# Kernel optimization log

Measured on AMD Instinct MI355X. Metric: run time of the kernel, lower is better.

The kernel has to match this reference:

```python
import jax, jax.numpy as jnp
import numpy as np

N, X_DIM, Z_DIM, H = 4096, 256, 128, 512
NUM_ACTIONS = 4
TEMPERATURE = 0.1


def _init_linear(key, fan_in, fan_out):
    kw, kb = jax.random.split(key)
    bound = 1.0 / np.sqrt(fan_in)
    W = jax.random.uniform(kw, (fan_in, fan_out), minval=-bound, maxval=bound, dtype=jnp.float32)
    b = jax.random.uniform(kb, (fan_out,), minval=-bound, maxval=bound, dtype=jnp.float32)
    return W, b


def setup_inputs() -> dict:
    key = jax.random.key(0)
    ks = jax.random.split(key, 9)
    s = jax.random.normal(ks[0], (N, X_DIM), dtype=jnp.float32)
    sp = jax.random.normal(ks[1], (N, X_DIM), dtype=jnp.float32)
    a = jax.random.randint(ks[2], (N,), 0, NUM_ACTIONS)
    a1h = jax.nn.one_hot(a, NUM_ACTIONS, dtype=jnp.float32)
    # phi: x_dim -> 512 -> 512 -> z_dim
    pW0, pb0 = _init_linear(ks[3], X_DIM, H)
    pW1, pb1 = _init_linear(ks[4], H, H)
    pW2, pb2 = _init_linear(ks[5], H, Z_DIM)
    # g: x_dim + 4 -> 512 -> 512 -> z_dim
    gW0, gb0 = _init_linear(ks[6], X_DIM + NUM_ACTIONS, H)
    gW1, gb1 = _init_linear(ks[7], H, H)
    gW2, gb2 = _init_linear(ks[8], H, Z_DIM)
    return {"s": s, "sp": sp, "a1h": a1h,
            "pW0": pW0, "pb0": pb0, "pW1": pW1, "pb1": pb1, "pW2": pW2, "pb2": pb2,
            "gW0": gW0, "gb0": gb0, "gW1": gW1, "gb1": gb1, "gW2": gW2, "gb2": gb2}


def _mlp(x, W0, b0, W1, b1, W2, b2):
    h = jax.nn.relu(x @ W0 + b0)
    h = jax.nn.relu(h @ W1 + b1)
    return h @ W2 + b2


def reference(s, sp, a1h, pW0, pb0, pW1, pb1, pW2, pb2, gW0, gb0, gW1, gb1, gW2, gb2):
    z = _mlp(s, pW0, pb0, pW1, pb1, pW2, pb2)                      # [N, D]
    zpos = _mlp(jnp.concatenate([sp, a1h], axis=-1), gW0, gb0, gW1, gb1, gW2, gb2)  # [N, D]
    # -||z_i - zpos_j||^2 / T via the GEMM trick (avoids the [N,N,D] diff tensor)
    sq_z = jnp.sum(z * z, axis=-1, keepdims=True)                  # [N, 1]
    sq_p = jnp.sum(zpos * zpos, axis=-1)                            # [N]
    logits = -(sq_z + sq_p[None, :] - 2.0 * z @ zpos.T) / TEMPERATURE  # [N, N]
    # cross-entropy with targets = arange(N): diagonal is the positive
    log_probs = jax.nn.log_softmax(logits, axis=-1)
    loss = -jnp.mean(jnp.diagonal(log_probs))
    return loss
```

## Files before the change

### kernel.cpp

```cpp
#include <hip/hip_runtime.h>
#include <math.h>

#define NR 4096
#define ZD 128
#define HD 512
#define NJR 32
#define INV_T 10.0f

typedef __attribute__((ext_vector_type(8))) short bf16x8;
typedef __attribute__((ext_vector_type(4))) short short4v;
typedef __attribute__((ext_vector_type(4))) float f32x4;

typedef const unsigned int __attribute__((address_space(1)))* gas_t;
typedef unsigned int __attribute__((address_space(3)))* las_t;

__device__ __forceinline__ unsigned short f2bf(float f) {
  union { float f; unsigned u; } v; v.f = f;
  unsigned r = v.u + 0x7fff + ((v.u >> 16) & 1);
  return (unsigned short)(r >> 16);
}
__device__ __forceinline__ float bf2f(unsigned short b) {
  union { unsigned u; float f; } v; v.u = ((unsigned)b) << 16;
  return v.f;
}


__global__ __launch_bounds__(256) void prep(
    const float* __restrict__ s, const float* __restrict__ sp,
    const float* __restrict__ a1h,
    unsigned short* __restrict__ Sb, unsigned short* __restrict__ SPb,
    int* __restrict__ aidx,
    const float* __restrict__ pW0, unsigned short* __restrict__ pW0t,
    const float* __restrict__ pW1, unsigned short* __restrict__ pW1t,
    const float* __restrict__ pW2, unsigned short* __restrict__ pW2t,
    const float* __restrict__ gW0, unsigned short* __restrict__ gW0t,
    const float* __restrict__ gW1, unsigned short* __restrict__ gW1t,
    const float* __restrict__ gW2, unsigned short* __restrict__ gW2t,
    float* __restrict__ out) {
  int b = blockIdx.x, tid = threadIdx.x;
  if (b < 16) {
    int r = b * 256 + tid;
    int a = 0;
#pragma unroll
    for (int j = 0; j < 4; ++j) if (a1h[(size_t)r * 4 + j] > 0.5f) a = j;
    aidx[r] = a;
    if (b == 0 && tid == 0) out[0] = 0.f;
    return;
  }
  const int idx8 = tid & 127;
  const int h = idx8 & 1, p = idx8 >> 1, hi = p >> 4, l15 = p & 15;
  if (b < 2064) {
    const float* src = (b < 1040) ? s : sp;
    unsigned short* dst = (b < 1040) ? Sb : SPb;
    int lb = (b < 1040) ? b - 16 : b - 1040;
    int s0 = lb * 2 + (tid >> 7);
    int rf = s0 >> 3, ks = s0 & 7;
    int row = rf * 16 + l15, c0 = ks * 32 + hi * 4 + h * 16;
    float4 v = *(const float4*)&src[(size_t)row * 256 + c0];
    short4v o = { (short)f2bf(v.x), (short)f2bf(v.y), (short)f2bf(v.z), (short)f2bf(v.w) };
    *(short4v*)((char*)dst + (size_t)s0 * 1024 + idx8 * 8) = o;
    return;
  }
  int local = b - 2064;
  const float* W; unsigned short* Wt; int N, ksh;
  if (local < 128)      { W = pW0; Wt = pW0t; N = 512; ksh = 3; }
  else if (local < 384) { W = pW1; Wt = pW1t; N = 512; ksh = 4; local -= 128; }
  else if (local < 448) { W = pW2; Wt = pW2t; N = 128; ksh = 4; local -= 384; }
  else if (local < 576) { W = gW0; Wt = gW0t; N = 512; ksh = 3; local -= 448; }
  else if (local < 832) { W = gW1; Wt = gW1t; N = 512; ksh = 4; local -= 576; }
  else                  { W = gW2; Wt = gW2t; N = 128; ksh = 4; local -= 832; }
  int s0 = local * 2 + (tid >> 7);
  int rf = s0 >> ksh, ks = s0 & ((1 << ksh) - 1);
  int n = rf * 16 + l15, k0 = ks * 32 + hi * 4 + h * 16;
  short4v o = { (short)f2bf(W[(size_t)(k0 + 0) * N + n]),
                (short)f2bf(W[(size_t)(k0 + 1) * N + n]),
                (short)f2bf(W[(size_t)(k0 + 2) * N + n]),
                (short)f2bf(W[(size_t)(k0 + 3) * N + n]) };
  *(short4v*)((char*)Wt + (size_t)s0 * 1024 + idx8 * 8) = o;
}

template <int BM, int K, bool RELU, bool GB, bool SQ>
__global__ __launch_bounds__(256) void gemm_p3(
    const unsigned short* __restrict__ A0, const unsigned short* __restrict__ A1,
    const unsigned short* __restrict__ W0, const unsigned short* __restrict__ W1,
    const float* __restrict__ b0, const float* __restrict__ b1,
    unsigned short* __restrict__ C0, unsigned short* __restrict__ C1,
    float* __restrict__ sqp2, int N,
    const int* __restrict__ aidx, const float* __restrict__ gW0f) {
  constexpr int KS = K >> 5;
  constexpr int NSTEP = K >> 6;
  constexpr int ABYTES = BM * 128;
  constexpr int BBYTES = 8192;
  constexpr int NA = BM >> 5;
  constexpr int WM_FR = BM >> 5;
  constexpr int V = NA + 2;
  __shared__ char lds[3 * (ABYTES + BBYTES)];
  char* AsB = lds;
  char* BsB = lds + 3 * ABYTES;

  const int tid = threadIdx.x, lane = tid & 63, w = tid >> 6;
  const int wm = w >> 1, wn = w & 1;
  const int z = blockIdx.z;
  const char* Ab = (const char*)(z ? A1 : A0);
  const char* Wb = (const char*)(z ? W1 : W0);
  const float* bias = z ? b1 : b0;
  char* Cb = (char*)(z ? C1 : C0);
  const int bm = blockIdx.x * BM, bn = blockIdx.y * 64;
  const int lane16 = lane * 16;

  auto stage = [&](int buf, int st) {
#pragma unroll
    for (int u = 0; u < NA; ++u) {
      const int sl = w * NA + u;
      const char* src = Ab + ((size_t)((bm >> 4) + (sl >> 1)) * KS + st * 2 + (sl & 1)) * 1024 + lane16;
      __builtin_amdgcn_global_load_lds((gas_t)src, (las_t)(AsB + buf * ABYTES + sl * 1024), 16, 0, 0);
    }
#pragma unroll
    for (int u = 0; u < 2; ++u) {
      const int sl = w * 2 + u;
      const char* src = Wb + ((size_t)((bn >> 4) + (sl >> 1)) * KS + st * 2 + (sl & 1)) * 1024 + lane16;
      __builtin_amdgcn_global_load_lds((gas_t)src, (las_t)(BsB + buf * BBYTES + sl * 1024), 16, 0, 0);
    }
  };

  f32x4 acc[WM_FR][2] = {};
  stage(0, 0);
  stage(1, 1);
#pragma unroll
  for (int st = 0; st < NSTEP; ++st) {
    const int buf = st % 3;
    if (st + 2 < NSTEP) {
      stage((st + 2) % 3, st + 2);
      if constexpr (V == 6) asm volatile("s_waitcnt vmcnt(12)" ::: "memory");
      else                  asm volatile("s_waitcnt vmcnt(8)" ::: "memory");
    } else if (st + 1 < NSTEP) {
      if constexpr (V == 6) asm volatile("s_waitcnt vmcnt(6)" ::: "memory");
      else                  asm volatile("s_waitcnt vmcnt(4)" ::: "memory");
    } else {
      asm volatile("s_waitcnt vmcnt(0)" ::: "memory");
    }
    __builtin_amdgcn_s_barrier();
#pragma unroll
    for (int kss = 0; kss < 2; ++kss) {
      bf16x8 af[WM_FR], bfv[2];
#pragma unroll
      for (int i = 0; i < WM_FR; ++i)
        af[i] = *(const bf16x8*)(AsB + buf * ABYTES + ((wm * WM_FR + i) * 2 + kss) * 1024 + lane16);
#pragma unroll
      for (int j = 0; j < 2; ++j)
        bfv[j] = *(const bf16x8*)(BsB + buf * BBYTES + ((wn * 2 + j) * 2 + kss) * 1024 + lane16);
#pragma unroll
      for (int i = 0; i < WM_FR; ++i)
#pragma unroll
        for (int j = 0; j < 2; ++j)
          acc[i][j] = __builtin_amdgcn_mfma_f32_16x16x32_bf16(bfv[j], af[i], acc[i][j], 0, 0, 0);
    }
    __builtin_amdgcn_s_barrier();
  }

  const int l15 = lane & 15, hi = lane >> 4;
  const int NS = N >> 5;
  const int row0 = bm + wm * (BM / 2);
  const int col0 = bn + wn * 32;
  float sq[WM_FR];
  int ar[WM_FR];
#pragma unroll
  for (int i = 0; i < WM_FR; ++i) { sq[i] = 0.f; ar[i] = 0; }
  if (GB && z == 1) {
#pragma unroll
    for (int i = 0; i < WM_FR; ++i) ar[i] = aidx[row0 + i * 16 + l15];
  }
  float4 bi0 = *(const float4*)&bias[col0 + hi * 4];
  float4 bi1 = *(const float4*)&bias[col0 + 16 + hi * 4];
#pragma unroll
  for (int i = 0; i < WM_FR; ++i) {
    const int rfC = (row0 >> 4) + i;
    float v[8] = { acc[i][0][0] + bi0.x, acc[i][0][1] + bi0.y,
                   acc[i][0][2] + bi0.z, acc[i][0][3] + bi0.w,
                   acc[i][1][0] + bi1.x, acc[i][1][1] + bi1.y,
                   acc[i][1][2] + bi1.z, acc[i][1][3] + bi1.w };
    if (GB && z == 1) {
      float4 g0 = *(const float4*)&gW0f[(size_t)(256 + ar[i]) * N + col0 + hi * 4];
      float4 g1 = *(const float4*)&gW0f[(size_t)(256 + ar[i]) * N + col0 + 16 + hi * 4];
      v[0] += g0.x; v[1] += g0.y; v[2] += g0.z; v[3] += g0.w;
      v[4] += g1.x; v[5] += g1.y; v[6] += g1.z; v[7] += g1.w;
    }
    bf16x8 r;
#pragma unroll
    for (int t = 0; t < 8; ++t) {
      float vv = RELU ? fmaxf(v[t], 0.f) : v[t];
      unsigned short cv = f2bf(vv);
      r[t] = (short)cv;
      if (SQ) { float vb = bf2f(cv); sq[i] += vb * vb; }
    }
    *(bf16x8*)(Cb + (size_t)(rfC * NS + (col0 >> 5)) * 1024 + lane16) = r;
  }
  if (SQ && z == 1) {
#pragma unroll
    for (int i = 0; i < WM_FR; ++i) {
      float t = sq[i];
      t += __shfl_xor(t, 16, 64);
      t += __shfl_xor(t, 32, 64);
      if (lane < 16) sqp2[(size_t)(col0 >> 5) * NR + row0 + i * 16 + lane] = t;
    }
  }
}

__global__ __launch_bounds__(256) void logits_fm(
    const unsigned short* __restrict__ Zb, const unsigned short* __restrict__ Zpb,
    const float* __restrict__ sqp2, float* __restrict__ wm_,
    float* __restrict__ wsum, float* __restrict__ wdiag) {
  const int tid = threadIdx.x, lane = tid & 63, w = tid >> 6;
  const int l15 = lane & 15, hi = lane >> 4;
  const int i0 = blockIdx.x * 128, jr = blockIdx.y;
  const int row32 = i0 + w * 32;
  const int jbase = jr * 128;
  const int lane16 = lane * 16;
  const char* Zc = (const char*)Zb;
  const char* Pc = (const char*)Zpb;

  bf16x8 afr[2][4];
#pragma unroll
  for (int rf = 0; rf < 2; ++rf)
#pragma unroll
    for (int ks = 0; ks < 4; ++ks)
      afr[rf][ks] = *(const bf16x8*)(Zc + (size_t)(((row32 >> 4) + rf) * 4 + ks) * 1024 + lane16);

  f32x4 acc[2][8] = {};
#pragma unroll
  for (int jf = 0; jf < 8; ++jf) {
    const size_t js = (size_t)((jbase >> 4) + jf) * 4;
#pragma unroll
    for (int ks = 0; ks < 4; ++ks) {
      bf16x8 bfv = *(const bf16x8*)(Pc + (js + ks) * 1024 + lane16);
      acc[0][jf] = __builtin_amdgcn_mfma_f32_16x16x32_bf16(bfv, afr[0][ks], acc[0][jf], 0, 0, 0);
      acc[1][jf] = __builtin_amdgcn_mfma_f32_16x16x32_bf16(bfv, afr[1][ks], acc[1][jf], 0, 0, 0);
    }
  }

#pragma unroll
  for (int rf = 0; rf < 2; ++rf) {
    const int grow = row32 + rf * 16 + l15;
    float mx = -INFINITY, dd = 0.f;
    bool hasd = false;
#pragma unroll
    for (int jf = 0; jf < 8; ++jf) {
      const int cb = jbase + jf * 16 + hi * 4;
      float4 q0 = *(const float4*)&sqp2[cb];
      float4 q1 = *(const float4*)&sqp2[NR + cb];
      float4 q2 = *(const float4*)&sqp2[2 * NR + cb];
      float4 q3 = *(const float4*)&sqp2[3 * NR + cb];
      float sp[4] = { q0.x + q1.x + q2.x + q3.x, q0.y + q1.y + q2.y + q3.y,
                      q0.z + q1.z + q2.z + q3.z, q0.w + q1.w + q2.w + q3.w };
#pragma unroll
      for (int e = 0; e < 4; ++e) {
        float lv = (2.f * acc[rf][jf][e] - sp[e]) * INV_T;
        acc[rf][jf][e] = lv;
        mx = fmaxf(mx, lv);
        if (cb + e == grow) { dd = lv; hasd = true; }
      }
    }
    mx = fmaxf(mx, __shfl_xor(mx, 16, 64));
    mx = fmaxf(mx, __shfl_xor(mx, 32, 64));
    float sum = 0.f;
#pragma unroll
    for (int jf = 0; jf < 8; ++jf)
#pragma unroll
      for (int e = 0; e < 4; ++e) sum += __expf(acc[rf][jf][e] - mx);
    sum += __shfl_xor(sum, 16, 64);
    sum += __shfl_xor(sum, 32, 64);
    if (hi == 0) {
      wm_[(size_t)jr * NR + grow] = mx;
      wsum[(size_t)jr * NR + grow] = sum;
    }
    if (hasd) wdiag[grow] = dd;
  }
}

__global__ __launch_bounds__(256) void finalize(const float* __restrict__ wm,
    const float* __restrict__ wsum, const float* __restrict__ wdiag,
    float* __restrict__ out) {
  int r = blockIdx.x * 256 + threadIdx.x;
  float mm = wm[r];
  float ss = wsum[r];
#pragma unroll
  for (int p = 1; p < NJR; ++p) {
    float mo = wm[(size_t)p * NR + r];
    float so = wsum[(size_t)p * NR + r];
    float mn = fmaxf(mm, mo);
    ss = ss * __expf(mm - mn) + so * __expf(mo - mn);
    mm = mn;
  }
  float loss_r = mm + logf(ss) - wdiag[r];
  float v = loss_r;
#pragma unroll
  for (int off = 32; off; off >>= 1) v += __shfl_xor(v, off, 64);
  __shared__ float partial[4];
  if ((threadIdx.x & 63) == 0) partial[threadIdx.x >> 6] = v;
  __syncthreads();
  if (threadIdx.x == 0)
    atomicAdd(out, (partial[0] + partial[1] + partial[2] + partial[3]) * (1.0f / (float)NR));
}

extern "C" void kernel_launch(void* const* d_in, const int* in_sizes, int n_in,
                              void* d_out, int out_size, void* d_ws, size_t ws_size,
                              hipStream_t stream) {
  const float* s   = (const float*)d_in[0];
  const float* sp  = (const float*)d_in[1];
  const float* a1h = (const float*)d_in[2];
  const float* pW0 = (const float*)d_in[3];
  const float* pb0 = (const float*)d_in[4];
  const float* pW1 = (const float*)d_in[5];
  const float* pb1 = (const float*)d_in[6];
  const float* pW2 = (const float*)d_in[7];
  const float* pb2 = (const float*)d_in[8];
  const float* gW0 = (const float*)d_in[9];
  const float* gb0 = (const float*)d_in[10];
  const float* gW1 = (const float*)d_in[11];
  const float* gb1 = (const float*)d_in[12];
  const float* gW2 = (const float*)d_in[13];
  const float* gb2 = (const float*)d_in[14];

  char* p = (char*)d_ws;
  unsigned short* Sb   = (unsigned short*)p; p += (size_t)NR * 256 * 2;
  unsigned short* SPb  = (unsigned short*)p; p += (size_t)NR * 256 * 2;
  unsigned short* H1   = (unsigned short*)p; p += (size_t)2 * NR * HD * 2;
  unsigned short* H2   = (unsigned short*)p; p += (size_t)2 * NR * HD * 2;
  unsigned short* Zall = (unsigned short*)p; p += (size_t)2 * NR * ZD * 2;
  unsigned short* pW0t = (unsigned short*)p; p += (size_t)256 * 512 * 2;
  unsigned short* pW1t = (unsigned short*)p; p += (size_t)512 * 512 * 2;
  unsigned short* pW2t = (unsigned short*)p; p += (size_t)512 * 128 * 2;
  unsigned short* gW0t = (unsigned short*)p; p += (size_t)256 * 512 * 2;
  unsigned short* gW1t = (unsigned short*)p; p += (size_t)512 * 512 * 2;
  unsigned short* gW2t = (unsigned short*)p; p += (size_t)512 * 128 * 2;
  float* sqp2 = (float*)p; p += (size_t)4 * NR * 4;
  float* wm   = (float*)p; p += (size_t)NJR * NR * 4;
  float* wsm  = (float*)p; p += (size_t)NJR * NR * 4;
  float* wdg  = (float*)p; p += (size_t)NR * 4;
  int*   aidx = (int*)p;  p += (size_t)NR * 4;

  unsigned short* H1g = H1 + (size_t)NR * HD;
  unsigned short* H2g = H2 + (size_t)NR * HD;
  unsigned short* Zb  = Zall;
  unsigned short* Zpb = Zall + (size_t)NR * ZD;

  dim3 blk(256);
  prep<<<2960, blk, 0, stream>>>(s, sp, a1h, Sb, SPb, aidx,
                                 pW0, pW0t, pW1, pW1t, pW2, pW2t,
                                 gW0, gW0t, gW1, gW1t, gW2, gW2t,
                                 (float*)d_out);

  gemm_p3<128, 256, true, true, false><<<dim3(32, 8, 2), blk, 0, stream>>>(
      Sb, SPb, pW0t, gW0t, pb0, gb0, H1, H1g, nullptr, 512, aidx, gW0);
  gemm_p3<128, 512, true, false, false><<<dim3(32, 8, 2), blk, 0, stream>>>(
      H1, H1g, pW1t, gW1t, pb1, gb1, H2, H2g, nullptr, 512, nullptr, nullptr);
  gemm_p3<64, 512, false, false, true><<<dim3(64, 2, 2), blk, 0, stream>>>(
      H2, H2g, pW2t, gW2t, pb2, gb2, Zb, Zpb, sqp2, 128, nullptr, nullptr);

  logits_fm<<<dim3(NR / 128, NJR), blk, 0, stream>>>(Zb, Zpb, sqp2, wm, wsm, wdg);
  finalize<<<NR / 256, blk, 0, stream>>>(wm, wsm, wdg, (float*)d_out);
}
```

Measured before the change: 54.47 us.

## Fuse three MLP GEMM layers into one kernel keeping hidden activations in LDS

Replaces the three per-layer GEMM launches with a single kernel in which each block processes 32 rows through all three layers. Hidden activations stay in shared memory instead of round-tripping through global H1/H2 buffers. Weights are streamed directly from global memory into registers with one-step register prefetch instead of the LDS triple-buffered pipeline. This removes launch overhead and intermediate global traffic, but every block rereads the full weight matrices from global/L2, with 256 blocks and larger per-wave register footprint.

```diff
diff --git a/kernel.cpp b/kernel.cpp
--- a/kernel.cpp
+++ b/kernel.cpp
@@ -2,7 +2,6 @@
 #include <math.h>
 
 #define NR 4096
-#define ZD 128
 #define HD 512
 #define NJR 32
 #define INV_T 10.0f
@@ -10,9 +9,6 @@
 typedef __attribute__((ext_vector_type(8))) short bf16x8;
 typedef __attribute__((ext_vector_type(4))) short short4v;
 typedef __attribute__((ext_vector_type(4))) float f32x4;
-
-typedef const unsigned int __attribute__((address_space(1)))* gas_t;
-typedef unsigned int __attribute__((address_space(3)))* las_t;
 
 __device__ __forceinline__ unsigned short f2bf(float f) {
   union { float f; unsigned u; } v; v.f = f;
@@ -79,129 +75,191 @@
   *(short4v*)((char*)Wt + (size_t)s0 * 1024 + idx8 * 8) = o;
 }
 
-template <int BM, int K, bool RELU, bool GB, bool SQ>
-__global__ __launch_bounds__(256) void gemm_p3(
-    const unsigned short* __restrict__ A0, const unsigned short* __restrict__ A1,
-    const unsigned short* __restrict__ W0, const unsigned short* __restrict__ W1,
-    const float* __restrict__ b0, const float* __restrict__ b1,
-    unsigned short* __restrict__ C0, unsigned short* __restrict__ C1,
-    float* __restrict__ sqp2, int N,
-    const int* __restrict__ aidx, const float* __restrict__ gW0f) {
-  constexpr int KS = K >> 5;
-  constexpr int NSTEP = K >> 6;
-  constexpr int ABYTES = BM * 128;
-  constexpr int BBYTES = 8192;
-  constexpr int NA = BM >> 5;
-  constexpr int WM_FR = BM >> 5;
-  constexpr int V = NA + 2;
-  __shared__ char lds[3 * (ABYTES + BBYTES)];
-  char* AsB = lds;
-  char* BsB = lds + 3 * ABYTES;
-
-  const int tid = threadIdx.x, lane = tid & 63, w = tid >> 6;
-  const int wm = w >> 1, wn = w & 1;
-  const int z = blockIdx.z;
-  const char* Ab = (const char*)(z ? A1 : A0);
-  const char* Wb = (const char*)(z ? W1 : W0);
-  const float* bias = z ? b1 : b0;
-  char* Cb = (char*)(z ? C1 : C0);
-  const int bm = blockIdx.x * BM, bn = blockIdx.y * 64;
+__global__ __launch_bounds__(256) void mlp_fused(
+    const unsigned short* __restrict__ Sb, const unsigned short* __restrict__ SPb,
+    const unsigned short* __restrict__ pW0t, const unsigned short* __restrict__ pW1t,
+    const unsigned short* __restrict__ pW2t,
+    const unsigned short* __restrict__ gW0t, const unsigned short* __restrict__ gW1t,
+    const unsigned short* __restrict__ gW2t,
+    const float* __restrict__ pb0, const float* __restrict__ pb1,
+    const float* __restrict__ pb2,
+    const float* __restrict__ gb0, const float* __restrict__ gb1,
+    const float* __restrict__ gb2,
+    unsigned short* __restrict__ Zb, unsigned short* __restrict__ Zpb,
+    float* __restrict__ sqp2, const int* __restrict__ aidx,
+    const float* __restrict__ gW0f) {
+  __shared__ __align__(1024) char Hs[32768];
+  const int tid = threadIdx.x, lane = tid & 63, wn = tid >> 6;
+  const int l15 = lane & 15, hi = lane >> 4;
+  const int z = blockIdx.y;
+  const int bm = blockIdx.x * 32;
   const int lane16 = lane * 16;
-
-  auto stage = [&](int buf, int st) {
-#pragma unroll
-    for (int u = 0; u < NA; ++u) {
-      const int sl = w * NA + u;
-      const char* src = Ab + ((size_t)((bm >> 4) + (sl >> 1)) * KS + st * 2 + (sl & 1)) * 1024 + lane16;
-      __builtin_amdgcn_global_load_lds((gas_t)src, (las_t)(AsB + buf * ABYTES + sl * 1024), 16, 0, 0);
-    }
-#pragma unroll
-    for (int u = 0; u < 2; ++u) {
-      const int sl = w * 2 + u;
-      const char* src = Wb + ((size_t)((bn >> 4) + (sl >> 1)) * KS + st * 2 + (sl & 1)) * 1024 + lane16;
-      __builtin_amdgcn_global_load_lds((gas_t)src, (las_t)(BsB + buf * BBYTES + sl * 1024), 16, 0, 0);
-    }
-  };
-
-  f32x4 acc[WM_FR][2] = {};
-  stage(0, 0);
-  stage(1, 1);
-#pragma unroll
-  for (int st = 0; st < NSTEP; ++st) {
-    const int buf = st % 3;
-    if (st + 2 < NSTEP) {
-      stage((st + 2) % 3, st + 2);
-      if constexpr (V == 6) asm volatile("s_waitcnt vmcnt(12)" ::: "memory");
-      else                  asm volatile("s_waitcnt vmcnt(8)" ::: "memory");
-    } else if (st + 1 < NSTEP) {
-      if constexpr (V == 6) asm volatile("s_waitcnt vmcnt(6)" ::: "memory");
-      else                  asm volatile("s_waitcnt vmcnt(4)" ::: "memory");
-    } else {
-      asm volatile("s_waitcnt vmcnt(0)" ::: "memory");
-    }
-    __builtin_amdgcn_s_barrier();
-#pragma unroll
-    for (int kss = 0; kss < 2; ++kss) {
-      bf16x8 af[WM_FR], bfv[2];
-#pragma unroll
-      for (int i = 0; i < WM_FR; ++i)
-        af[i] = *(const bf16x8*)(AsB + buf * ABYTES + ((wm * WM_FR + i) * 2 + kss) * 1024 + lane16);
-#pragma unroll
-      for (int j = 0; j < 2; ++j)
-        bfv[j] = *(const bf16x8*)(BsB + buf * BBYTES + ((wn * 2 + j) * 2 + kss) * 1024 + lane16);
-#pragma unroll
-      for (int i = 0; i < WM_FR; ++i)
-#pragma unroll
-        for (int j = 0; j < 2; ++j)
-          acc[i][j] = __builtin_amdgcn_mfma_f32_16x16x32_bf16(bfv[j], af[i], acc[i][j], 0, 0, 0);
-    }
-    __builtin_amdgcn_s_barrier();
-  }
-
-  const int l15 = lane & 15, hi = lane >> 4;
-  const int NS = N >> 5;
-  const int row0 = bm + wm * (BM / 2);
-  const int col0 = bn + wn * 32;
-  float sq[WM_FR];
-  int ar[WM_FR];
-#pragma unroll
-  for (int i = 0; i < WM_FR; ++i) { sq[i] = 0.f; ar[i] = 0; }
-  if (GB && z == 1) {
-#pragma unroll
-    for (int i = 0; i < WM_FR; ++i) ar[i] = aidx[row0 + i * 16 + l15];
-  }
-  float4 bi0 = *(const float4*)&bias[col0 + hi * 4];
-  float4 bi1 = *(const float4*)&bias[col0 + 16 + hi * 4];
-#pragma unroll
-  for (int i = 0; i < WM_FR; ++i) {
-    const int rfC = (row0 >> 4) + i;
-    float v[8] = { acc[i][0][0] + bi0.x, acc[i][0][1] + bi0.y,
-                   acc[i][0][2] + bi0.z, acc[i][0][3] + bi0.w,
-                   acc[i][1][0] + bi1.x, acc[i][1][1] + bi1.y,
-                   acc[i][1][2] + bi1.z, acc[i][1][3] + bi1.w };
-    if (GB && z == 1) {
-      float4 g0 = *(const float4*)&gW0f[(size_t)(256 + ar[i]) * N + col0 + hi * 4];
-      float4 g1 = *(const float4*)&gW0f[(size_t)(256 + ar[i]) * N + col0 + 16 + hi * 4];
-      v[0] += g0.x; v[1] += g0.y; v[2] += g0.z; v[3] += g0.w;
-      v[4] += g1.x; v[5] += g1.y; v[6] += g1.z; v[7] += g1.w;
-    }
-    bf16x8 r;
-#pragma unroll
-    for (int t = 0; t < 8; ++t) {
-      float vv = RELU ? fmaxf(v[t], 0.f) : v[t];
-      unsigned short cv = f2bf(vv);
-      r[t] = (short)cv;
-      if (SQ) { float vb = bf2f(cv); sq[i] += vb * vb; }
-    }
-    *(bf16x8*)(Cb + (size_t)(rfC * NS + (col0 >> 5)) * 1024 + lane16) = r;
-  }
-  if (SQ && z == 1) {
-#pragma unroll
-    for (int i = 0; i < WM_FR; ++i) {
-      float t = sq[i];
-      t += __shfl_xor(t, 16, 64);
-      t += __shfl_xor(t, 32, 64);
-      if (lane < 16) sqp2[(size_t)(col0 >> 5) * NR + row0 + i * 16 + lane] = t;
+  const char* Ab  = (const char*)(z ? SPb : Sb);
+  const char* W0b = (const char*)(z ? gW0t : pW0t);
+  const char* W1b = (const char*)(z ? gW1t : pW1t);
+  const char* W2b = (const char*)(z ? gW2t : pW2t);
+  const float* b0 = z ? gb0 : pb0;
+  const float* b1 = z ? gb1 : pb1;
+  const float* b2 = z ? gb2 : pb2;
+  char* Cb = (char*)(z ? Zpb : Zb);
+
+  int ar[2];
+  ar[0] = aidx[bm + l15];
+  ar[1] = aidx[bm + 16 + l15];
+
+  {
+    f32x4 acc[2][8] = {};
+    bf16x8 bcur[8], acur[2];
+#pragma unroll
+    for (int jf = 0; jf < 8; ++jf)
+      bcur[jf] = *(const bf16x8*)(W0b + (size_t)((wn * 8 + jf) * 8) * 1024 + lane16);
+#pragma unroll
+    for (int rf = 0; rf < 2; ++rf)
+      acur[rf] = *(const bf16x8*)(Ab + (size_t)(((bm >> 4) + rf) * 8) * 1024 + lane16);
+#pragma unroll
+    for (int ks = 0; ks < 8; ++ks) {
+      bf16x8 bnx[8], anx[2];
+      if (ks < 7) {
+#pragma unroll
+        for (int jf = 0; jf < 8; ++jf)
+          bnx[jf] = *(const bf16x8*)(W0b + (size_t)((wn * 8 + jf) * 8 + ks + 1) * 1024 + lane16);
+#pragma unroll
+        for (int rf = 0; rf < 2; ++rf)
+          anx[rf] = *(const bf16x8*)(Ab + (size_t)(((bm >> 4) + rf) * 8 + ks + 1) * 1024 + lane16);
+      }
+#pragma unroll
+      for (int rf = 0; rf < 2; ++rf)
+#pragma unroll
+        for (int jf = 0; jf < 8; ++jf)
+          acc[rf][jf] = __builtin_amdgcn_mfma_f32_16x16x32_bf16(bcur[jf], acur[rf], acc[rf][jf], 0, 0, 0);
+      if (ks < 7) {
+#pragma unroll
+        for (int jf = 0; jf < 8; ++jf) bcur[jf] = bnx[jf];
+        acur[0] = anx[0]; acur[1] = anx[1];
+      }
+    }
+#pragma unroll
+    for (int rf = 0; rf < 2; ++rf)
+#pragma unroll
+      for (int q = 0; q < 4; ++q) {
+        const int col0 = wn * 128 + q * 32;
+        float4 bi0 = *(const float4*)&b0[col0 + hi * 4];
+        float4 bi1 = *(const float4*)&b0[col0 + 16 + hi * 4];
+        float v[8] = { acc[rf][2 * q][0] + bi0.x, acc[rf][2 * q][1] + bi0.y,
+                       acc[rf][2 * q][2] + bi0.z, acc[rf][2 * q][3] + bi0.w,
+                       acc[rf][2 * q + 1][0] + bi1.x, acc[rf][2 * q + 1][1] + bi1.y,
+                       acc[rf][2 * q + 1][2] + bi1.z, acc[rf][2 * q + 1][3] + bi1.w };
+        if (z == 1) {
+          float4 g0 = *(const float4*)&gW0f[(size_t)(256 + ar[rf]) * 512 + col0 + hi * 4];
+          float4 g1 = *(const float4*)&gW0f[(size_t)(256 + ar[rf]) * 512 + col0 + 16 + hi * 4];
+          v[0] += g0.x; v[1] += g0.y; v[2] += g0.z; v[3] += g0.w;
+          v[4] += g1.x; v[5] += g1.y; v[6] += g1.z; v[7] += g1.w;
+        }
+        bf16x8 r;
+#pragma unroll
+        for (int t = 0; t < 8; ++t) r[t] = (short)f2bf(fmaxf(v[t], 0.f));
+        *(bf16x8*)(Hs + ((rf * 16 + wn * 4 + q) * 1024) + lane16) = r;
+      }
+  }
+  __syncthreads();
+
+  {
+    f32x4 acc[2][8] = {};
+    bf16x8 bcur[8];
+#pragma unroll
+    for (int jf = 0; jf < 8; ++jf)
+      bcur[jf] = *(const bf16x8*)(W1b + (size_t)((wn * 8 + jf) * 16) * 1024 + lane16);
+#pragma unroll
+    for (int ks = 0; ks < 16; ++ks) {
+      bf16x8 bnx[8];
+      if (ks < 15) {
+#pragma unroll
+        for (int jf = 0; jf < 8; ++jf)
+          bnx[jf] = *(const bf16x8*)(W1b + (size_t)((wn * 8 + jf) * 16 + ks + 1) * 1024 + lane16);
+      }
+      bf16x8 a0 = *(const bf16x8*)(Hs + ((0 * 16 + ks) * 1024) + lane16);
+      bf16x8 a1 = *(const bf16x8*)(Hs + ((1 * 16 + ks) * 1024) + lane16);
+#pragma unroll
+      for (int jf = 0; jf < 8; ++jf) {
+        acc[0][jf] = __builtin_amdgcn_mfma_f32_16x16x32_bf16(bcur[jf], a0, acc[0][jf], 0, 0, 0);
+        acc[1][jf] = __builtin_amdgcn_mfma_f32_16x16x32_bf16(bcur[jf], a1, acc[1][jf], 0, 0, 0);
+      }
+      if (ks < 15) {
+#pragma unroll
+        for (int jf = 0; jf < 8; ++jf) bcur[jf] = bnx[jf];
+      }
+    }
+    __syncthreads();
+#pragma unroll
+    for (int rf = 0; rf < 2; ++rf)
+#pragma unroll
+      for (int q = 0; q < 4; ++q) {
+        const int col0 = wn * 128 + q * 32;
+        float4 bi0 = *(const float4*)&b1[col0 + hi * 4];
+        float4 bi1 = *(const float4*)&b1[col0 + 16 + hi * 4];
+        float v[8] = { acc[rf][2 * q][0] + bi0.x, acc[rf][2 * q][1] + bi0.y,
+                       acc[rf][2 * q][2] + bi0.z, acc[rf][2 * q][3] + bi0.w,
+                       acc[rf][2 * q + 1][0] + bi1.x, acc[rf][2 * q + 1][1] + bi1.y,
+                       acc[rf][2 * q + 1][2] + bi1.z, acc[rf][2 * q + 1][3] + bi1.w };
+        bf16x8 r;
+#pragma unroll
+        for (int t = 0; t < 8; ++t) r[t] = (short)f2bf(fmaxf(v[t], 0.f));
+        *(bf16x8*)(Hs + ((rf * 16 + wn * 4 + q) * 1024) + lane16) = r;
+      }
+  }
+  __syncthreads();
+
+  {
+    f32x4 acc[2][2] = {};
+    bf16x8 bcur[2];
+#pragma unroll
+    for (int fn = 0; fn < 2; ++fn)
+      bcur[fn] = *(const bf16x8*)(W2b + (size_t)((wn * 2 + fn) * 16) * 1024 + lane16);
+#pragma unroll
+    for (int ks = 0; ks < 16; ++ks) {
+      bf16x8 bnx[2];
+      if (ks < 15) {
+#pragma unroll
+        for (int fn = 0; fn < 2; ++fn)
+          bnx[fn] = *(const bf16x8*)(W2b + (size_t)((wn * 2 + fn) * 16 + ks + 1) * 1024 + lane16);
+      }
+      bf16x8 a0 = *(const bf16x8*)(Hs + ((0 * 16 + ks) * 1024) + lane16);
+      bf16x8 a1 = *(const bf16x8*)(Hs + ((1 * 16 + ks) * 1024) + lane16);
+#pragma unroll
+      for (int fn = 0; fn < 2; ++fn) {
+        acc[0][fn] = __builtin_amdgcn_mfma_f32_16x16x32_bf16(bcur[fn], a0, acc[0][fn], 0, 0, 0);
+        acc[1][fn] = __builtin_amdgcn_mfma_f32_16x16x32_bf16(bcur[fn], a1, acc[1][fn], 0, 0, 0);
+      }
+      if (ks < 15) { bcur[0] = bnx[0]; bcur[1] = bnx[1]; }
+    }
+    const int col0 = wn * 32;
+    float4 bi0 = *(const float4*)&b2[col0 + hi * 4];
+    float4 bi1 = *(const float4*)&b2[col0 + 16 + hi * 4];
+    float sq[2] = {0.f, 0.f};
+#pragma unroll
+    for (int rf = 0; rf < 2; ++rf) {
+      float v[8] = { acc[rf][0][0] + bi0.x, acc[rf][0][1] + bi0.y,
+                     acc[rf][0][2] + bi0.z, acc[rf][0][3] + bi0.w,
+                     acc[rf][1][0] + bi1.x, acc[rf][1][1] + bi1.y,
+                     acc[rf][1][2] + bi1.z, acc[rf][1][3] + bi1.w };
+      bf16x8 r;
+#pragma unroll
+      for (int t = 0; t < 8; ++t) {
+        unsigned short cv = f2bf(v[t]);
+        r[t] = (short)cv;
+        float vb = bf2f(cv);
+        sq[rf] += vb * vb;
+      }
+      *(bf16x8*)(Cb + (size_t)((((bm >> 4) + rf) * 4 + wn) * 1024) + lane16) = r;
+    }
+    if (z == 1) {
+#pragma unroll
+      for (int rf = 0; rf < 2; ++rf) {
+        float t = sq[rf];
+        t += __shfl_xor(t, 16, 64);
+        t += __shfl_xor(t, 32, 64);
+        if (lane < 16) sqp2[(size_t)wn * NR + bm + rf * 16 + lane] = t;
+      }
     }
   }
 }
@@ -324,9 +382,7 @@
   char* p = (char*)d_ws;
   unsigned short* Sb   = (unsigned short*)p; p += (size_t)NR * 256 * 2;
   unsigned short* SPb  = (unsigned short*)p; p += (size_t)NR * 256 * 2;
-  unsigned short* H1   = (unsigned short*)p; p += (size_t)2 * NR * HD * 2;
-  unsigned short* H2   = (unsigned short*)p; p += (size_t)2 * NR * HD * 2;
-  unsigned short* Zall = (unsigned short*)p; p += (size_t)2 * NR * ZD * 2;
+  unsigned short* Zall = (unsigned short*)p; p += (size_t)2 * NR * 128 * 2;
   unsigned short* pW0t = (unsigned short*)p; p += (size_t)256 * 512 * 2;
   unsigned short* pW1t = (unsigned short*)p; p += (size_t)512 * 512 * 2;
   unsigned short* pW2t = (unsigned short*)p; p += (size_t)512 * 128 * 2;
@@ -339,10 +395,8 @@
   float* wdg  = (float*)p; p += (size_t)NR * 4;
   int*   aidx = (int*)p;  p += (size_t)NR * 4;
 
-  unsigned short* H1g = H1 + (size_t)NR * HD;
-  unsigned short* H2g = H2 + (size_t)NR * HD;
   unsigned short* Zb  = Zall;
-  unsigned short* Zpb = Zall + (size_t)NR * ZD;
+  unsigned short* Zpb = Zall + (size_t)NR * 128;
 
   dim3 blk(256);
   prep<<<2960, blk, 0, stream>>>(s, sp, a1h, Sb, SPb, aidx,
@@ -350,12 +404,10 @@
                                  gW0, gW0t, gW1, gW1t, gW2, gW2t,
                                  (float*)d_out);
 
-  gemm_p3<128, 256, true, true, false><<<dim3(32, 8, 2), blk, 0, stream>>>(
-      Sb, SPb, pW0t, gW0t, pb0, gb0, H1, H1g, nullptr, 512, aidx, gW0);
-  gemm_p3<128, 512, true, false, false><<<dim3(32, 8, 2), blk, 0, stream>>>(
-      H1, H1g, pW1t, gW1t, pb1, gb1, H2, H2g, nullptr, 512, nullptr, nullptr);
-  gemm_p3<64, 512, false, false, true><<<dim3(64, 2, 2), blk, 0, stream>>>(
-      H2, H2g, pW2t, gW2t, pb2, gb2, Zb, Zpb, sqp2, 128, nullptr, nullptr);
+  mlp_fused<<<dim3(NR / 32, 2), blk, 0, stream>>>(
+      Sb, SPb, pW0t, pW1t, pW2t, gW0t, gW1t, gW2t,
+      pb0, pb1, pb2, gb0, gb1, gb2,
+      Zb, Zpb, sqp2, aidx, gW0);
 
   logits_fm<<<dim3(NR / 128, NJR), blk, 0, stream>>>(Zb, Zpb, sqp2, wm, wsm, wdg);
   finalize<<<NR / 256, blk, 0, stream>>>(wm, wsm, wdg, (float*)d_out);
```

Measured after the change: 71.19 us. 30.7% more time.

## Switch MLP GEMMs to smaller double-buffered tiles and atomic squared-norm accumulation

Applied to the files above, without the earlier changes.

The MLP GEMM kernel now uses generic BM/BN tiles with double buffering in place of triple buffering. Layers 0 and 1 drop from 128x64 to 64x64 tiles and layer 2 from 64x64 to 64x32, doubling the block count per launch to improve occupancy and wave balance. The per-column-slab squared-norm partials are replaced by atomicAdd into one zeroed array, so the logits kernel reads one value per column instead of summing four. The trade-off is less data reuse per tile, a shallower prefetch pipeline, and atomic contention on the norm buffer.

```diff
diff --git a/kernel.cpp b/kernel.cpp
--- a/kernel.cpp
+++ b/kernel.cpp
@@ -2,7 +2,6 @@
 #include <math.h>
 
 #define NR 4096
-#define ZD 128
 #define HD 512
 #define NJR 32
 #define INV_T 10.0f
@@ -29,7 +28,7 @@
     const float* __restrict__ s, const float* __restrict__ sp,
     const float* __restrict__ a1h,
     unsigned short* __restrict__ Sb, unsigned short* __restrict__ SPb,
-    int* __restrict__ aidx,
+    int* __restrict__ aidx, float* __restrict__ sqp,
     const float* __restrict__ pW0, unsigned short* __restrict__ pW0t,
     const float* __restrict__ pW1, unsigned short* __restrict__ pW1t,
     const float* __restrict__ pW2, unsigned short* __restrict__ pW2t,
@@ -44,6 +43,7 @@
 #pragma unroll
     for (int j = 0; j < 4; ++j) if (a1h[(size_t)r * 4 + j] > 0.5f) a = j;
     aidx[r] = a;
+    sqp[r] = 0.f;
     if (b == 0 && tid == 0) out[0] = 0.f;
     return;
   }
@@ -79,24 +79,24 @@
   *(short4v*)((char*)Wt + (size_t)s0 * 1024 + idx8 * 8) = o;
 }
 
-template <int BM, int K, bool RELU, bool GB, bool SQ>
-__global__ __launch_bounds__(256) void gemm_p3(
+template <int BM, int BN, int K, bool RELU, bool GB, bool SQ>
+__global__ __launch_bounds__(256) void gemm_db(
     const unsigned short* __restrict__ A0, const unsigned short* __restrict__ A1,
     const unsigned short* __restrict__ W0, const unsigned short* __restrict__ W1,
     const float* __restrict__ b0, const float* __restrict__ b1,
     unsigned short* __restrict__ C0, unsigned short* __restrict__ C1,
-    float* __restrict__ sqp2, int N,
+    float* __restrict__ sqp, int N,
     const int* __restrict__ aidx, const float* __restrict__ gW0f) {
   constexpr int KS = K >> 5;
   constexpr int NSTEP = K >> 6;
-  constexpr int ABYTES = BM * 128;
-  constexpr int BBYTES = 8192;
-  constexpr int NA = BM >> 5;
-  constexpr int WM_FR = BM >> 5;
-  constexpr int V = NA + 2;
-  __shared__ char lds[3 * (ABYTES + BBYTES)];
-  char* AsB = lds;
-  char* BsB = lds + 3 * ABYTES;
+  constexpr int ABY = BM * 128;
+  constexpr int BBY = BN * 128;
+  constexpr int RFW = BM >> 5;
+  constexpr int FNW = BN >> 5;
+  constexpr int V = RFW + FNW;
+  __shared__ char lds[2 * (ABY + BBY)];
+  char* As = lds;
+  char* Bs = lds + 2 * ABY;
 
   const int tid = threadIdx.x, lane = tid & 63, w = tid >> 6;
   const int wm = w >> 1, wn = w & 1;
@@ -105,54 +105,50 @@
   const char* Wb = (const char*)(z ? W1 : W0);
   const float* bias = z ? b1 : b0;
   char* Cb = (char*)(z ? C1 : C0);
-  const int bm = blockIdx.x * BM, bn = blockIdx.y * 64;
+  const int bm = blockIdx.x * BM, bn = blockIdx.y * BN;
   const int lane16 = lane * 16;
 
   auto stage = [&](int buf, int st) {
 #pragma unroll
-    for (int u = 0; u < NA; ++u) {
-      const int sl = w * NA + u;
+    for (int u = 0; u < RFW; ++u) {
+      const int sl = w * RFW + u;
       const char* src = Ab + ((size_t)((bm >> 4) + (sl >> 1)) * KS + st * 2 + (sl & 1)) * 1024 + lane16;
-      __builtin_amdgcn_global_load_lds((gas_t)src, (las_t)(AsB + buf * ABYTES + sl * 1024), 16, 0, 0);
-    }
-#pragma unroll
-    for (int u = 0; u < 2; ++u) {
-      const int sl = w * 2 + u;
+      __builtin_amdgcn_global_load_lds((gas_t)src, (las_t)(As + buf * ABY + sl * 1024), 16, 0, 0);
+    }
+#pragma unroll
+    for (int u = 0; u < FNW; ++u) {
+      const int sl = w * FNW + u;
       const char* src = Wb + ((size_t)((bn >> 4) + (sl >> 1)) * KS + st * 2 + (sl & 1)) * 1024 + lane16;
-      __builtin_amdgcn_global_load_lds((gas_t)src, (las_t)(BsB + buf * BBYTES + sl * 1024), 16, 0, 0);
+      __builtin_amdgcn_global_load_lds((gas_t)src, (las_t)(Bs + buf * BBY + sl * 1024), 16, 0, 0);
     }
   };
 
-  f32x4 acc[WM_FR][2] = {};
+  f32x4 acc[RFW][FNW] = {};
   stage(0, 0);
-  stage(1, 1);
 #pragma unroll
   for (int st = 0; st < NSTEP; ++st) {
-    const int buf = st % 3;
-    if (st + 2 < NSTEP) {
-      stage((st + 2) % 3, st + 2);
-      if constexpr (V == 6) asm volatile("s_waitcnt vmcnt(12)" ::: "memory");
-      else                  asm volatile("s_waitcnt vmcnt(8)" ::: "memory");
-    } else if (st + 1 < NSTEP) {
-      if constexpr (V == 6) asm volatile("s_waitcnt vmcnt(6)" ::: "memory");
-      else                  asm volatile("s_waitcnt vmcnt(4)" ::: "memory");
+    const int buf = st & 1;
+    if (st + 1 < NSTEP) {
+      stage(buf ^ 1, st + 1);
+      if constexpr (V == 4) asm volatile("s_waitcnt vmcnt(4)" ::: "memory");
+      else                  asm volatile("s_waitcnt vmcnt(3)" ::: "memory");
     } else {
       asm volatile("s_waitcnt vmcnt(0)" ::: "memory");
     }
     __builtin_amdgcn_s_barrier();
 #pragma unroll
     for (int kss = 0; kss < 2; ++kss) {
-      bf16x8 af[WM_FR], bfv[2];
-#pragma unroll
-      for (int i = 0; i < WM_FR; ++i)
-        af[i] = *(const bf16x8*)(AsB + buf * ABYTES + ((wm * WM_FR + i) * 2 + kss) * 1024 + lane16);
-#pragma unroll
-      for (int j = 0; j < 2; ++j)
-        bfv[j] = *(const bf16x8*)(BsB + buf * BBYTES + ((wn * 2 + j) * 2 + kss) * 1024 + lane16);
-#pragma unroll
-      for (int i = 0; i < WM_FR; ++i)
-#pragma unroll
-        for (int j = 0; j < 2; ++j)
+      bf16x8 af[RFW], bfv[FNW];
+#pragma unroll
+      for (int i = 0; i < RFW; ++i)
+        af[i] = *(const bf16x8*)(As + buf * ABY + ((wm * RFW + i) * 2 + kss) * 1024 + lane16);
+#pragma unroll
+      for (int j = 0; j < FNW; ++j)
+        bfv[j] = *(const bf16x8*)(Bs + buf * BBY + ((wn * FNW + j) * 2 + kss) * 1024 + lane16);
+#pragma unroll
+      for (int i = 0; i < RFW; ++i)
+#pragma unroll
+        for (int j = 0; j < FNW; ++j)
           acc[i][j] = __builtin_amdgcn_mfma_f32_16x16x32_bf16(bfv[j], af[i], acc[i][j], 0, 0, 0);
     }
     __builtin_amdgcn_s_barrier();
@@ -160,55 +156,74 @@
 
   const int l15 = lane & 15, hi = lane >> 4;
   const int NS = N >> 5;
-  const int row0 = bm + wm * (BM / 2);
-  const int col0 = bn + wn * 32;
-  float sq[WM_FR];
-  int ar[WM_FR];
-#pragma unroll
-  for (int i = 0; i < WM_FR; ++i) { sq[i] = 0.f; ar[i] = 0; }
+  const int row0 = bm + wm * (RFW * 16);
+  const int col0 = bn + wn * (FNW * 16);
+  int ar[RFW];
+#pragma unroll
+  for (int i = 0; i < RFW; ++i) ar[i] = 0;
   if (GB && z == 1) {
 #pragma unroll
-    for (int i = 0; i < WM_FR; ++i) ar[i] = aidx[row0 + i * 16 + l15];
-  }
-  float4 bi0 = *(const float4*)&bias[col0 + hi * 4];
-  float4 bi1 = *(const float4*)&bias[col0 + 16 + hi * 4];
-#pragma unroll
-  for (int i = 0; i < WM_FR; ++i) {
-    const int rfC = (row0 >> 4) + i;
-    float v[8] = { acc[i][0][0] + bi0.x, acc[i][0][1] + bi0.y,
-                   acc[i][0][2] + bi0.z, acc[i][0][3] + bi0.w,
-                   acc[i][1][0] + bi1.x, acc[i][1][1] + bi1.y,
-                   acc[i][1][2] + bi1.z, acc[i][1][3] + bi1.w };
-    if (GB && z == 1) {
-      float4 g0 = *(const float4*)&gW0f[(size_t)(256 + ar[i]) * N + col0 + hi * 4];
-      float4 g1 = *(const float4*)&gW0f[(size_t)(256 + ar[i]) * N + col0 + 16 + hi * 4];
-      v[0] += g0.x; v[1] += g0.y; v[2] += g0.z; v[3] += g0.w;
-      v[4] += g1.x; v[5] += g1.y; v[6] += g1.z; v[7] += g1.w;
-    }
-    bf16x8 r;
-#pragma unroll
-    for (int t = 0; t < 8; ++t) {
-      float vv = RELU ? fmaxf(v[t], 0.f) : v[t];
-      unsigned short cv = f2bf(vv);
-      r[t] = (short)cv;
-      if (SQ) { float vb = bf2f(cv); sq[i] += vb * vb; }
-    }
-    *(bf16x8*)(Cb + (size_t)(rfC * NS + (col0 >> 5)) * 1024 + lane16) = r;
-  }
-  if (SQ && z == 1) {
-#pragma unroll
-    for (int i = 0; i < WM_FR; ++i) {
-      float t = sq[i];
-      t += __shfl_xor(t, 16, 64);
-      t += __shfl_xor(t, 32, 64);
-      if (lane < 16) sqp2[(size_t)(col0 >> 5) * NR + row0 + i * 16 + lane] = t;
+    for (int i = 0; i < RFW; ++i) ar[i] = aidx[row0 + i * 16 + l15];
+  }
+  if constexpr (FNW == 2) {
+    float4 bi0 = *(const float4*)&bias[col0 + hi * 4];
+    float4 bi1 = *(const float4*)&bias[col0 + 16 + hi * 4];
+#pragma unroll
+    for (int i = 0; i < RFW; ++i) {
+      const int rfC = (row0 >> 4) + i;
+      float v[8] = { acc[i][0][0] + bi0.x, acc[i][0][1] + bi0.y,
+                     acc[i][0][2] + bi0.z, acc[i][0][3] + bi0.w,
+                     acc[i][1][0] + bi1.x, acc[i][1][1] + bi1.y,
+                     acc[i][1][2] + bi1.z, acc[i][1][3] + bi1.w };
+      if (GB && z == 1) {
+        float4 g0 = *(const float4*)&gW0f[(size_t)(256 + ar[i]) * N + col0 + hi * 4];
+        float4 g1 = *(const float4*)&gW0f[(size_t)(256 + ar[i]) * N + col0 + 16 + hi * 4];
+        v[0] += g0.x; v[1] += g0.y; v[2] += g0.z; v[3] += g0.w;
+        v[4] += g1.x; v[5] += g1.y; v[6] += g1.z; v[7] += g1.w;
+      }
+      bf16x8 r;
+#pragma unroll
+      for (int t = 0; t < 8; ++t) {
+        float vv = RELU ? fmaxf(v[t], 0.f) : v[t];
+        r[t] = (short)f2bf(vv);
+      }
+      *(bf16x8*)(Cb + (size_t)(rfC * NS + (col0 >> 5)) * 1024 + lane16) = r;
+    }
+  } else {
+    float4 bi0 = *(const float4*)&bias[col0 + hi * 4];
+    float sq[RFW];
+#pragma unroll
+    for (int i = 0; i < RFW; ++i) sq[i] = 0.f;
+#pragma unroll
+    for (int i = 0; i < RFW; ++i) {
+      const int rfC = (row0 >> 4) + i;
+      float v[4] = { acc[i][0][0] + bi0.x, acc[i][0][1] + bi0.y,
+                     acc[i][0][2] + bi0.z, acc[i][0][3] + bi0.w };
+      short4v r;
+#pragma unroll
+      for (int t = 0; t < 4; ++t) {
+        float vv = RELU ? fmaxf(v[t], 0.f) : v[t];
+        unsigned short cv = f2bf(vv);
+        r[t] = (short)cv;
+        if (SQ) { float vb = bf2f(cv); sq[i] += vb * vb; }
+      }
+      *(short4v*)(Cb + (size_t)(rfC * NS + (bn >> 5)) * 1024 + lane16 + wn * 8) = r;
+    }
+    if (SQ && z == 1) {
+#pragma unroll
+      for (int i = 0; i < RFW; ++i) {
+        float t = sq[i];
+        t += __shfl_xor(t, 16, 64);
+        t += __shfl_xor(t, 32, 64);
+        if (lane < 16) atomicAdd(&sqp[row0 + i * 16 + lane], t);
+      }
     }
   }
 }
 
 __global__ __launch_bounds__(256) void logits_fm(
     const unsigned short* __restrict__ Zb, const unsigned short* __restrict__ Zpb,
-    const float* __restrict__ sqp2, float* __restrict__ wm_,
+    const float* __restrict__ sqp, float* __restrict__ wm_,
     float* __restrict__ wsum, float* __restrict__ wdiag) {
   const int tid = threadIdx.x, lane = tid & 63, w = tid >> 6;
   const int l15 = lane & 15, hi = lane >> 4;
@@ -246,12 +261,8 @@
 #pragma unroll
     for (int jf = 0; jf < 8; ++jf) {
       const int cb = jbase + jf * 16 + hi * 4;
-      float4 q0 = *(const float4*)&sqp2[cb];
-      float4 q1 = *(const float4*)&sqp2[NR + cb];
-      float4 q2 = *(const float4*)&sqp2[2 * NR + cb];
-      float4 q3 = *(const float4*)&sqp2[3 * NR + cb];
-      float sp[4] = { q0.x + q1.x + q2.x + q3.x, q0.y + q1.y + q2.y + q3.y,
-                      q0.z + q1.z + q2.z + q3.z, q0.w + q1.w + q2.w + q3.w };
+      float4 q = *(const float4*)&sqp[cb];
+      float sp[4] = { q.x, q.y, q.z, q.w };
 #pragma unroll
       for (int e = 0; e < 4; ++e) {
         float lv = (2.f * acc[rf][jf][e] - sp[e]) * INV_T;
@@ -326,14 +337,14 @@
   unsigned short* SPb  = (unsigned short*)p; p += (size_t)NR * 256 * 2;
   unsigned short* H1   = (unsigned short*)p; p += (size_t)2 * NR * HD * 2;
   unsigned short* H2   = (unsigned short*)p; p += (size_t)2 * NR * HD * 2;
-  unsigned short* Zall = (unsigned short*)p; p += (size_t)2 * NR * ZD * 2;
+  unsigned short* Zall = (unsigned short*)p; p += (size_t)2 * NR * 128 * 2;
   unsigned short* pW0t = (unsigned short*)p; p += (size_t)256 * 512 * 2;
   unsigned short* pW1t = (unsigned short*)p; p += (size_t)512 * 512 * 2;
   unsigned short* pW2t = (unsigned short*)p; p += (size_t)512 * 128 * 2;
   unsigned short* gW0t = (unsigned short*)p; p += (size_t)256 * 512 * 2;
   unsigned short* gW1t = (unsigned short*)p; p += (size_t)512 * 512 * 2;
   unsigned short* gW2t = (unsigned short*)p; p += (size_t)512 * 128 * 2;
-  float* sqp2 = (float*)p; p += (size_t)4 * NR * 4;
+  float* sqp  = (float*)p; p += (size_t)NR * 4;
   float* wm   = (float*)p; p += (size_t)NJR * NR * 4;
   float* wsm  = (float*)p; p += (size_t)NJR * NR * 4;
   float* wdg  = (float*)p; p += (size_t)NR * 4;
@@ -342,21 +353,21 @@
   unsigned short* H1g = H1 + (size_t)NR * HD;
   unsigned short* H2g = H2 + (size_t)NR * HD;
   unsigned short* Zb  = Zall;
-  unsigned short* Zpb = Zall + (size_t)NR * ZD;
+  unsigned short* Zpb = Zall + (size_t)NR * 128;
 
   dim3 blk(256);
-  prep<<<2960, blk, 0, stream>>>(s, sp, a1h, Sb, SPb, aidx,
+  prep<<<2960, blk, 0, stream>>>(s, sp, a1h, Sb, SPb, aidx, sqp,
                                  pW0, pW0t, pW1, pW1t, pW2, pW2t,
                                  gW0, gW0t, gW1, gW1t, gW2, gW2t,
                                  (float*)d_out);
 
-  gemm_p3<128, 256, true, true, false><<<dim3(32, 8, 2), blk, 0, stream>>>(
+  gemm_db<64, 64, 256, true, true, false><<<dim3(64, 8, 2), blk, 0, stream>>>(
       Sb, SPb, pW0t, gW0t, pb0, gb0, H1, H1g, nullptr, 512, aidx, gW0);
-  gemm_p3<128, 512, true, false, false><<<dim3(32, 8, 2), blk, 0, stream>>>(
+  gemm_db<64, 64, 512, true, false, false><<<dim3(64, 8, 2), blk, 0, stream>>>(
       H1, H1g, pW1t, gW1t, pb1, gb1, H2, H2g, nullptr, 512, nullptr, nullptr);
-  gemm_p3<64, 512, false, false, true><<<dim3(64, 2, 2), blk, 0, stream>>>(
-      H2, H2g, pW2t, gW2t, pb2, gb2, Zb, Zpb, sqp2, 128, nullptr, nullptr);
-
-  logits_fm<<<dim3(NR / 128, NJR), blk, 0, stream>>>(Zb, Zpb, sqp2, wm, wsm, wdg);
+  gemm_db<64, 32, 512, false, false, true><<<dim3(64, 4, 2), blk, 0, stream>>>(
+      H2, H2g, pW2t, gW2t, pb2, gb2, Zb, Zpb, sqp, 128, nullptr, nullptr);
+
+  logits_fm<<<dim3(NR / 128, NJR), blk, 0, stream>>>(Zb, Zpb, sqp, wm, wsm, wdg);
   finalize<<<NR / 256, blk, 0, stream>>>(wm, wsm, wdg, (float*)d_out);
 }
```

Measured after the change: 57.32 us. +5.2%, slower.
